# Kernel optimization log

Hardware: AMD Instinct MI355X
Metric: run time of the kernel (lower is better)

The kernel has to match this reference:

```python
import jax, jax.numpy as jnp
import numpy as np

B, N, C = 4, 1024, 1024
H = 16
D = C // H
FF = 4 * C
EPS = 1e-5


def setup_inputs() -> dict:
    key = jax.random.key(0)
    ks = jax.random.split(key, 16)
    s = 0.02
    return {
        "x": jax.random.normal(ks[0], (B, N, C), jnp.float32),
        "c": jax.random.normal(ks[1], (B, C), jnp.float32),
        "node_mask": jax.random.randint(ks[2], (B, N), 0, 2) > 0,
        "qkv_w": jax.random.normal(ks[3], (C, 3 * C), jnp.float32) * s,
        "proj_w": jax.random.normal(ks[4], (C, C), jnp.float32) * s,
        "proj_b": jnp.zeros((C,), jnp.float32),
        "fc1_w": jax.random.normal(ks[5], (C, FF), jnp.float32) * s,
        "fc1_b": jnp.zeros((FF,), jnp.float32),
        "fc2_w": jax.random.normal(ks[6], (FF, C), jnp.float32) * s,
        "fc2_b": jnp.zeros((C,), jnp.float32),
        "ada1_w": jax.random.normal(ks[7], (C, C), jnp.float32) * s,
        "ada1_b": jnp.zeros((C,), jnp.float32),
        "ada2_w": jax.random.normal(ks[8], (C, 6 * C), jnp.float32) * s,
        "ada2_b": jnp.zeros((6 * C,), jnp.float32),
    }


def _layernorm(x):
    # LayerNorm without affine params (elementwise_affine=False), eps=1e-5
    mu = jnp.mean(x, axis=-1, keepdims=True)
    var = jnp.mean(jnp.square(x - mu), axis=-1, keepdims=True)
    return (x - mu) * jax.lax.rsqrt(var + EPS)


def _modulate(x, shift, scale):
    return x * (1.0 + scale[:, None, :]) + shift[:, None, :]


def _attention(x, node_mask, qkv_w, proj_w, proj_b):
    b, n, c = x.shape
    qkv = (x @ qkv_w).reshape(b, n, 3, H, D)
    q, k, v = jnp.moveaxis(qkv, 2, 0)          # each [b, n, H, D]
    q = q.transpose(0, 2, 1, 3)                # [b, H, n, D]
    k = k.transpose(0, 2, 1, 3)
    v = v.transpose(0, 2, 1, 3)
    scale = D ** -0.5
    scores = jnp.einsum("bhnd,bhmd->bhnm", q, k) * scale
    mask = node_mask[:, None, None, :]          # key mask [b,1,1,n]
    scores = jnp.where(mask, scores, -jnp.inf)
    attn = jax.nn.softmax(scores, axis=-1)
    out = jnp.einsum("bhnm,bhmd->bhnd", attn, v)
    out = out.transpose(0, 2, 1, 3).reshape(b, n, c)
    return out @ proj_w + proj_b


def _mlp(x, fc1_w, fc1_b, fc2_w, fc2_b):
    h = jax.nn.gelu(x @ fc1_w + fc1_b, approximate=False)
    return h @ fc2_w + fc2_b


def reference(x, c, node_mask, qkv_w, proj_w, proj_b, fc1_w, fc1_b,
              fc2_w, fc2_b, ada1_w, ada1_b, ada2_w, ada2_b):
    # adaLN: Linear -> SiLU -> Linear -> 6 chunks along feature dim
    ada = jax.nn.silu(c @ ada1_w + ada1_b) @ ada2_w + ada2_b
    (shift_msa, scale_msa, gate_msa,
     shift_mlp, scale_mlp, gate_mlp) = jnp.split(ada, 6, axis=1)

    attn_out = _attention(x, node_mask, qkv_w, proj_w, proj_b)
    x = x + gate_msa[:, None, :] * _modulate(_layernorm(attn_out), shift_msa, scale_msa)

    mlp_out = _mlp(x, fc1_w, fc1_b, fc2_w, fc2_b)
    x = x + gate_mlp[:, None, :] * _modulate(_layernorm(mlp_out), shift_mlp, scale_mlp)
    return x
```

## Files before the change

kernel.cpp:

```cpp
#include <hip/hip_runtime.h>

typedef unsigned short u16;
typedef __attribute__((ext_vector_type(8))) short short8;
typedef __attribute__((ext_vector_type(8))) unsigned short u16x8;
typedef __attribute__((ext_vector_type(4))) unsigned short u16x4;
typedef __attribute__((ext_vector_type(4))) float f32x4;

#define DEVINL __device__ __forceinline__
#define SGB0 __builtin_amdgcn_sched_barrier(0)

DEVINL u16 f2b(float f) {
    union { float f; unsigned u; } a; a.f = f;
    unsigned r = a.u + 0x7FFFu + ((a.u >> 16) & 1u);
    return (u16)(r >> 16);
}
DEVINL float b2f(u16 h) {
    union { unsigned u; float f; } a; a.u = ((unsigned)h) << 16;
    return a.f;
}

DEVINL void gload16(const void* g, void* l) {
    __builtin_amdgcn_global_load_lds(
        (const __attribute__((address_space(1))) void*)g,
        (__attribute__((address_space(3))) void*)l, 16, 0, 0);
}

__global__ void detect_mask(const unsigned char* __restrict__ m, int nbytes, int* __restrict__ flag) {
    __shared__ int any;
    if (threadIdx.x == 0) any = 0;
    __syncthreads();
    int loc = 0;
    for (int i = threadIdx.x; i < nbytes; i += 256)
        if ((i & 3) && m[i]) loc = 1;
    if (loc) atomicOr(&any, 1);
    __syncthreads();
    if (threadIdx.x == 0) *flag = any;
}

__global__ __launch_bounds__(256) void f32_to_bf16(const float* __restrict__ in, u16* __restrict__ out, int n4) {
    int i = blockIdx.x * 256 + threadIdx.x;
    if (i >= n4) return;
    float4 v = ((const float4*)in)[i];
    u16x4 o = { f2b(v.x), f2b(v.y), f2b(v.z), f2b(v.w) };
    *(u16x4*)(out + (size_t)i * 4) = o;
}

__global__ __launch_bounds__(256) void transpose_bf16(const float* __restrict__ W, u16* __restrict__ WT, int K, int N) {
    __shared__ float tile[32][33];
    int tx = threadIdx.x, ty = threadIdx.y;
    int n0 = blockIdx.x * 32, k0 = blockIdx.y * 32;
#pragma unroll
    for (int i = 0; i < 4; i++)
        tile[ty + i * 8][tx] = W[(size_t)(k0 + ty + i * 8) * N + n0 + tx];
    __syncthreads();
#pragma unroll
    for (int i = 0; i < 4; i++)
        WT[(size_t)(n0 + ty + i * 8) * K + k0 + tx] = f2b(tile[tx][ty + i * 8]);
}

__global__ __launch_bounds__(256) void transpose_v(const u16* __restrict__ qkv, u16* __restrict__ vtg) {
    __shared__ u16 tile[64][72];
    const int bh = blockIdx.x & 63, nt = blockIdx.x >> 6;
    const int b = bh >> 4, h = bh & 15;
    const int t = threadIdx.x;
    const int r = t >> 3, c = (t & 7) << 3;
#pragma unroll
    for (int i = 0; i < 2; i++) {
        int rr = r + i * 32;
        *(u16x8*)&tile[rr][c] =
            *(const u16x8*)&qkv[(size_t)(b * 1024 + nt * 64 + rr) * 3072 + 2048 + h * 64 + c];
    }
    __syncthreads();
#pragma unroll
    for (int i = 0; i < 2; i++) {
        int d = r + i * 32;
        u16x8 o;
#pragma unroll
        for (int e = 0; e < 8; e++) o[e] = tile[c + e][d];
        *(u16x8*)&vtg[(size_t)bh * 65536 + (size_t)d * 1024 + nt * 64 + c] = o;
    }
}

template <int KRLOG2>
__global__ __launch_bounds__(256) void gemv_partial(
    const float* __restrict__ h, const float* __restrict__ w,
    float* __restrict__ part, int N, int K) {
    constexpr int KR = 1 << KRLOG2;
    constexpr int KR4 = KR >> 2;
    __shared__ float hs[4 * KR];
    __shared__ float red[256 * 16];
    const int t = threadIdx.x, wv = t >> 6, l = t & 63;
    const int j4 = blockIdx.x * 256 + l * 4;
    const int kb = blockIdx.y << KRLOG2;
    for (int idx = t; idx < 4 * KR; idx += 256) {
        int b = idx >> KRLOG2, kk = idx & (KR - 1);
        hs[idx] = h[b * K + kb + kk];
    }
    __syncthreads();
    float acc[4][4];
#pragma unroll
    for (int b = 0; b < 4; b++)
#pragma unroll
        for (int c = 0; c < 4; c++) acc[b][c] = 0.f;
    const float* wp = w + (size_t)(kb + wv * KR4) * N + j4;
#pragma unroll
    for (int i = 0; i < KR4; i++) {
        float4 wf = *(const float4*)(wp + (size_t)i * N);
        int kk = wv * KR4 + i;
#pragma unroll
        for (int b = 0; b < 4; b++) {
            float hv = hs[(b << KRLOG2) + kk];
            acc[b][0] += hv * wf.x;
            acc[b][1] += hv * wf.y;
            acc[b][2] += hv * wf.z;
            acc[b][3] += hv * wf.w;
        }
    }
#pragma unroll
    for (int b = 0; b < 4; b++)
#pragma unroll
        for (int c = 0; c < 4; c++)
            red[t * 16 + b * 4 + c] = acc[b][c];
    __syncthreads();
    if (t < 64) {
#pragma unroll
        for (int b = 0; b < 4; b++) {
            float4 s;
            s.x = red[l * 16 + b * 4 + 0] + red[(l + 64) * 16 + b * 4 + 0] + red[(l + 128) * 16 + b * 4 + 0] + red[(l + 192) * 16 + b * 4 + 0];
            s.y = red[l * 16 + b * 4 + 1] + red[(l + 64) * 16 + b * 4 + 1] + red[(l + 128) * 16 + b * 4 + 1] + red[(l + 192) * 16 + b * 4 + 1];
            s.z = red[l * 16 + b * 4 + 2] + red[(l + 64) * 16 + b * 4 + 2] + red[(l + 128) * 16 + b * 4 + 2] + red[(l + 192) * 16 + b * 4 + 2];
            s.w = red[l * 16 + b * 4 + 3] + red[(l + 64) * 16 + b * 4 + 3] + red[(l + 128) * 16 + b * 4 + 3] + red[(l + 192) * 16 + b * 4 + 3];
            *(float4*)&part[(size_t)(blockIdx.y * 4 + b) * N + j4] = s;
        }
    }
}

template <int SILU>
__global__ __launch_bounds__(256) void gemv_reduce(
    const float* __restrict__ part, const float* __restrict__ bias,
    float* __restrict__ out, int N, int NK) {
    int gid = blockIdx.x * 256 + threadIdx.x;
    int b = gid / N, j = gid - b * N;
    float s = bias[j];
    for (int i = 0; i < NK; i++) s += part[(size_t)(i * 4 + b) * N + j];
    if (SILU) s = s / (1.f + __expf(-s));
    out[gid] = s;
}

template <int EPI>
__global__ __launch_bounds__(256) void gemm_bt64(
    const u16* __restrict__ A, const u16* __restrict__ B, const float* __restrict__ bias,
    float* __restrict__ Cf, u16* __restrict__ Cb, int M, int N, int lda, int Ksub) {
    __shared__ u16 As[2][8192];
    __shared__ u16 Bs[2][8192];
    const int t = threadIdx.x;
    const int w = t >> 6, l = t & 63;
    const int l15 = l & 15, lg = l >> 4;
    const int nTN = N >> 7;
    const int ntiles = (M >> 7) * nTN;
    const int sk = blockIdx.x / ntiles;
    int tb = blockIdx.x - sk * ntiles;
    tb = (tb & 7) * (ntiles >> 3) + (tb >> 3);
    const int tm = tb / nTN, tn = tb - tm * nTN;
    const int row0 = tm << 7, col0 = tn << 7;
    const int wr = (w >> 1) << 6, wc = (w & 1) << 6;
    const int k_begin = sk * Ksub;

    const int rA = t >> 3;
    const int cswz = ((t & 7) ^ (rA & 7)) << 3;
    const u16* gA = A + (size_t)(row0 + rA) * lda + cswz + k_begin;
    const u16* gB = B + (size_t)(col0 + rA) * lda + cswz + k_begin;
    const int rsw = l15 & 7;

    f32x4 acc[4][4];
#pragma unroll
    for (int i = 0; i < 4; i++)
#pragma unroll
        for (int j = 0; j < 4; j++) acc[i][j] = (f32x4){0.f, 0.f, 0.f, 0.f};

    const int nsteps = Ksub >> 6;

#pragma unroll
    for (int j = 0; j < 4; j++) {
        gload16(gA + (size_t)j * 32 * lda, As[0] + j * 2048 + w * 512);
        gload16(gB + (size_t)j * 32 * lda, Bs[0] + j * 2048 + w * 512);
    }
#pragma unroll
    for (int j = 0; j < 4; j++) {
        gload16(gA + (size_t)j * 32 * lda + 64, As[1] + j * 2048 + w * 512);
        gload16(gB + (size_t)j * 32 * lda + 64, Bs[1] + j * 2048 + w * 512);
    }
    asm volatile("s_waitcnt vmcnt(8)" ::: "memory");
    SGB0;
    __builtin_amdgcn_s_barrier();
    SGB0;

    for (int it = 0; it < nsteps; ++it) {
        const int cur = it & 1;
        short8 af[2][4], bfr[2][4];
#pragma unroll
        for (int ks = 0; ks < 2; ks++) {
            const int chunk = ((ks << 2) + lg) ^ rsw;
#pragma unroll
            for (int mi = 0; mi < 4; mi++)
                af[ks][mi] = *(const short8*)&As[cur][((wr + mi * 16 + l15) << 6) + (chunk << 3)];
#pragma unroll
            for (int ni = 0; ni < 4; ni++)
                bfr[ks][ni] = *(const short8*)&Bs[cur][((wc + ni * 16 + l15) << 6) + (chunk << 3)];
        }
        asm volatile("s_waitcnt lgkmcnt(0)" ::: "memory");
        SGB0;
        __builtin_amdgcn_s_barrier();
        SGB0;
        if (it + 2 < nsteps) {
            const int k0 = (it + 2) << 6;
#pragma unroll
            for (int j = 0; j < 4; j++) {
                gload16(gA + (size_t)j * 32 * lda + k0, As[cur] + j * 2048 + w * 512);
                gload16(gB + (size_t)j * 32 * lda + k0, Bs[cur] + j * 2048 + w * 512);
            }
        }
        __builtin_amdgcn_s_setprio(1);
#pragma unroll
        for (int ks = 0; ks < 2; ks++)
#pragma unroll
            for (int mi = 0; mi < 4; mi++)
#pragma unroll
                for (int ni = 0; ni < 4; ni++)
                    acc[mi][ni] = __builtin_amdgcn_mfma_f32_16x16x32_bf16(af[ks][mi], bfr[ks][ni], acc[mi][ni], 0, 0, 0);
        __builtin_amdgcn_s_setprio(0);
        if (it + 1 < nsteps) {
            if (it + 2 < nsteps) asm volatile("s_waitcnt vmcnt(8)" ::: "memory");
            else                 asm volatile("s_waitcnt vmcnt(0)" ::: "memory");
            SGB0;
            __builtin_amdgcn_s_barrier();
            SGB0;
        }
    }

    float* Cfp = Cf ? Cf + (size_t)sk * M * N : nullptr;
    u16* Cbp = Cb ? Cb + (size_t)sk * M * N : nullptr;
#pragma unroll
    for (int mi = 0; mi < 4; mi++) {
#pragma unroll
        for (int ni = 0; ni < 4; ni++) {
#pragma unroll
            for (int j = 0; j < 4; j++) {
                int r = row0 + wr + mi * 16 + (lg << 2) + j;
                int c = col0 + wc + ni * 16 + l15;
                float v = acc[mi][ni][j];
                if (EPI == 0) {
                    Cbp[(size_t)r * N + c] = f2b(v);
                } else if (EPI == 2) {
                    float vv = v + bias[c];
                    float g = 0.5f * vv * (1.f + erff(vv * 0.70710678118f));
                    Cbp[(size_t)r * N + c] = f2b(g);
                } else {
                    Cfp[(size_t)r * N + c] = v;
                }
            }
        }
    }
}

__global__ __launch_bounds__(256) void attn_kernel(
    const u16* __restrict__ qkv, const u16* __restrict__ vtg,
    const unsigned char* __restrict__ maskb,
    const int* __restrict__ flagp, u16* __restrict__ out) {
    __shared__ u16 Qs[64 * 64];
    __shared__ u16 Ks[64 * 64];
    __shared__ u16 Vt[64 * 64];
    __shared__ u16 Ps[64 * 64];
    __shared__ float maskf[64];
    __shared__ float alpha_lds[64];
    __shared__ float lst_lds[64];

    int bi = (int)blockIdx.x;
    bi = (bi & 7) * 128 + (bi >> 3);
    const int qt = bi & 15, h = (bi >> 4) & 15, b = bi >> 8;
    const int t = threadIdx.x, w = t >> 6, l = t & 63;
    const int l15 = l & 15, lg = l >> 4;
    const int rsw = l15 & 7;
    const int flag = *flagp;
    const int q0 = qt << 6;
    const int bh = b * 16 + h;

    const int sr = t >> 3, sc = t & 7;
#pragma unroll
    for (int i = 0; i < 2; i++) {
        int r = sr + i * 32;
        u16x8 v = *(const u16x8*)&qkv[(size_t)(b * 1024 + q0 + r) * 3072 + h * 64 + sc * 8];
        u16x8 o;
#pragma unroll
        for (int e = 0; e < 8; e++) o[e] = f2b(b2f(v[e]) * 0.125f);
        *(u16x8*)&Qs[r * 64 + ((sc ^ (r & 7)) << 3)] = o;
    }

    f32x4 O[4];
#pragma unroll
    for (int nd = 0; nd < 4; nd++) O[nd] = (f32x4){0.f, 0.f, 0.f, 0.f};
    float mst = -1e30f, lst = 0.f;

    u16x8 kreg[2], vreg[2];
    float mnext;
    {
#pragma unroll
        for (int i = 0; i < 2; i++) {
            kreg[i] = *(const u16x8*)&qkv[(size_t)(b * 1024 + sr + i * 32) * 3072 + h * 64 + 1024 + sc * 8];
            vreg[i] = *(const u16x8*)&vtg[(size_t)bh * 65536 + (size_t)(sr + i * 32) * 1024 + sc * 8];
        }
        int gi = b * 1024 + (t & 63);
        bool ms = flag ? (maskb[gi] != 0) : (((const int*)maskb)[gi] != 0);
        mnext = ms ? 1.f : 0.f;
    }

    for (int kt = 0; kt < 16; kt++) {
        __syncthreads();
#pragma unroll
        for (int i = 0; i < 2; i++) {
            int r = sr + i * 32;
            *(u16x8*)&Ks[r * 64 + ((sc ^ (r & 7)) << 3)] = kreg[i];
            *(u16x8*)&Vt[r * 64 + ((sc ^ (r & 7)) << 3)] = vreg[i];
        }
        if (t < 64) maskf[t] = mnext;
        __syncthreads();
        if (kt < 15) {
            const int kn = (kt + 1) << 6;
#pragma unroll
            for (int i = 0; i < 2; i++) {
                kreg[i] = *(const u16x8*)&qkv[(size_t)(b * 1024 + kn + sr + i * 32) * 3072 + h * 64 + 1024 + sc * 8];
                vreg[i] = *(const u16x8*)&vtg[(size_t)bh * 65536 + (size_t)(sr + i * 32) * 1024 + kn + sc * 8];
            }
            int gi = b * 1024 + kn + (t & 63);
            bool ms = flag ? (maskb[gi] != 0) : (((const int*)maskb)[gi] != 0);
            mnext = ms ? 1.f : 0.f;
        }

        f32x4 S[4];
#pragma unroll
        for (int mi = 0; mi < 4; mi++) S[mi] = (f32x4){0.f, 0.f, 0.f, 0.f};
        __builtin_amdgcn_s_setprio(1);
#pragma unroll
        for (int ks = 0; ks < 2; ks++) {
            const int chunk = (((ks << 2) + lg) ^ rsw) << 3;
            short8 bq = *(const short8*)&Qs[(w * 16 + l15) * 64 + chunk];
#pragma unroll
            for (int mi = 0; mi < 4; mi++) {
                short8 ak = *(const short8*)&Ks[(mi * 16 + l15) * 64 + chunk];
                S[mi] = __builtin_amdgcn_mfma_f32_16x16x32_bf16(ak, bq, S[mi], 0, 0, 0);
            }
        }
        __builtin_amdgcn_s_setprio(0);

        float pm = -1e30f;
#pragma unroll
        for (int mi = 0; mi < 4; mi++) {
            f32x4 mk = *(const f32x4*)&maskf[mi * 16 + (lg << 2)];
#pragma unroll
            for (int j = 0; j < 4; j++) {
                float xv = (mk[j] > 0.f) ? S[mi][j] : -1e30f;
                S[mi][j] = xv;
                pm = fmaxf(pm, xv);
            }
        }
        pm = fmaxf(pm, __shfl_xor(pm, 16));
        pm = fmaxf(pm, __shfl_xor(pm, 32));

        bool skip = __all(pm <= mst + 8.f);
        float alpha = 1.f;
        if (!skip) {
            float mn = fmaxf(mst, pm);
            alpha = __expf(mst - mn);
            mst = mn;
        }

        float psum = 0.f;
        const int prow = w * 16 + l15;
#pragma unroll
        for (int mi = 0; mi < 4; mi++) {
            f32x4 mk = *(const f32x4*)&maskf[mi * 16 + (lg << 2)];
            u16x4 v4;
#pragma unroll
            for (int j = 0; j < 4; j++) {
                float p = __expf(S[mi][j] - mst) * mk[j];
                psum += p;
                v4[j] = f2b(p);
            }
            int ch = ((mi * 2 + (lg >> 1)) ^ rsw);
            *(u16x4*)&Ps[prow * 64 + (ch << 3) + ((lg & 1) << 2)] = v4;
        }
        psum += __shfl_xor(psum, 16);
        psum += __shfl_xor(psum, 32);
        lst = lst * alpha + psum;

        if (!skip) {
            if (lg == 0) alpha_lds[w * 16 + l15] = alpha;
            f32x4 af = *(const f32x4*)&alpha_lds[w * 16 + (lg << 2)];
#pragma unroll
            for (int nd = 0; nd < 4; nd++)
#pragma unroll
                for (int j = 0; j < 4; j++) O[nd][j] *= af[j];
        }

        __builtin_amdgcn_s_setprio(1);
#pragma unroll
        for (int ks = 0; ks < 2; ks++) {
            const int chunk = (((ks << 2) + lg) ^ rsw) << 3;
            short8 pa = *(const short8*)&Ps[(w * 16 + l15) * 64 + chunk];
#pragma unroll
            for (int nd = 0; nd < 4; nd++) {
                short8 bv = *(const short8*)&Vt[(nd * 16 + l15) * 64 + chunk];
                O[nd] = __builtin_amdgcn_mfma_f32_16x16x32_bf16(pa, bv, O[nd], 0, 0, 0);
            }
        }
        __builtin_amdgcn_s_setprio(0);
    }

    if (lg == 0) lst_lds[w * 16 + l15] = lst;
    f32x4 lf = *(const f32x4*)&lst_lds[w * 16 + (lg << 2)];
#pragma unroll
    for (int nd = 0; nd < 4; nd++)
#pragma unroll
        for (int j = 0; j < 4; j++) {
            int r = b * 1024 + q0 + w * 16 + (lg << 2) + j;
            int c = h * 64 + nd * 16 + l15;
            out[(size_t)r * 1024 + c] = f2b(O[nd][j] / lf[j]);
        }
}

template <int BF>
__global__ __launch_bounds__(256) void ln_mod_res2(
    const void* __restrict__ s0, const void* __restrict__ s1, const float* __restrict__ bias,
    const float* __restrict__ resid, const float* __restrict__ ada, int oS, int oC, int oG,
    float* __restrict__ outf, u16* __restrict__ outb) {
    __shared__ float red[8];
    const int row = blockIdx.x, t = threadIdx.x, b = row >> 10;
    const float4 bv = ((const float4*)bias)[t];
    float4 v;
    if (BF) {
        u16x4 a0 = *(const u16x4*)((const u16*)s0 + (size_t)row * 1024 + t * 4);
        u16x4 a1 = *(const u16x4*)((const u16*)s1 + (size_t)row * 1024 + t * 4);
        v.x = b2f(a0[0]) + b2f(a1[0]) + bv.x;
        v.y = b2f(a0[1]) + b2f(a1[1]) + bv.y;
        v.z = b2f(a0[2]) + b2f(a1[2]) + bv.z;
        v.w = b2f(a0[3]) + b2f(a1[3]) + bv.w;
    } else {
        float4 a0 = ((const float4*)((const float*)s0 + (size_t)row * 1024))[t];
        float4 a1 = ((const float4*)((const float*)s1 + (size_t)row * 1024))[t];
        v.x = a0.x + a1.x + bv.x;
        v.y = a0.y + a1.y + bv.y;
        v.z = a0.z + a1.z + bv.z;
        v.w = a0.w + a1.w + bv.w;
    }
    float s = v.x + v.y + v.z + v.w;
    float q = v.x * v.x + v.y * v.y + v.z * v.z + v.w * v.w;
#pragma unroll
    for (int off = 32; off >= 1; off >>= 1) {
        s += __shfl_down(s, off);
        q += __shfl_down(q, off);
    }
    if ((t & 63) == 0) { red[(t >> 6) * 2] = s; red[(t >> 6) * 2 + 1] = q; }
    __syncthreads();
    float sum = red[0] + red[2] + red[4] + red[6];
    float sq = red[1] + red[3] + red[5] + red[7];
    float mu = sum * (1.f / 1024.f);
    float var = sq * (1.f / 1024.f) - mu * mu;
    float rinv = rsqrtf(var + 1e-5f);
    const float* ad = ada + b * 6144;
    const float4 rv = ((const float4*)(resid + (size_t)row * 1024))[t];
    const float4 sc = ((const float4*)(ad + oC))[t];
    const float4 sh = ((const float4*)(ad + oS))[t];
    const float4 gt = ((const float4*)(ad + oG))[t];
    float4 o;
    o.x = rv.x + gt.x * ((v.x - mu) * rinv * (1.f + sc.x) + sh.x);
    o.y = rv.y + gt.y * ((v.y - mu) * rinv * (1.f + sc.y) + sh.y);
    o.z = rv.z + gt.z * ((v.z - mu) * rinv * (1.f + sc.z) + sh.z);
    o.w = rv.w + gt.w * ((v.w - mu) * rinv * (1.f + sc.w) + sh.w);
    ((float4*)(outf + (size_t)row * 1024))[t] = o;
    if (outb) {
        u16x4 ob = { f2b(o.x), f2b(o.y), f2b(o.z), f2b(o.w) };
        *(u16x4*)(outb + (size_t)row * 1024 + t * 4) = ob;
    }
}

extern "C" void kernel_launch(void* const* d_in, const int* in_sizes, int n_in,
                              void* d_out, int out_size, void* d_ws, size_t ws_size,
                              hipStream_t stream) {
    (void)in_sizes; (void)n_in; (void)out_size; (void)ws_size;
    const float* x = (const float*)d_in[0];
    const float* cvec = (const float*)d_in[1];
    const unsigned char* maskb = (const unsigned char*)d_in[2];
    const float* qkv_w = (const float*)d_in[3];
    const float* proj_w = (const float*)d_in[4];
    const float* proj_b = (const float*)d_in[5];
    const float* fc1_w = (const float*)d_in[6];
    const float* fc1_b = (const float*)d_in[7];
    const float* fc2_w = (const float*)d_in[8];
    const float* fc2_b = (const float*)d_in[9];
    const float* ada1_w = (const float*)d_in[10];
    const float* ada1_b = (const float*)d_in[11];
    const float* ada2_w = (const float*)d_in[12];
    const float* ada2_b = (const float*)d_in[13];
    float* outp = (float*)d_out;

    char* ws = (char*)d_ws;
    size_t off = 0;
    auto nxt = [&](size_t bytes) { size_t r = off; off += (bytes + 255) & ~(size_t)255; return r; };
    u16* qkvwT  = (u16*)(ws + nxt(3072ull * 1024 * 2));
    u16* projwT = (u16*)(ws + nxt(1024ull * 1024 * 2));
    u16* fc1wT  = (u16*)(ws + nxt(4096ull * 1024 * 2));
    u16* fc2wT  = (u16*)(ws + nxt(1024ull * 4096 * 2));
    float* adah = (float*)(ws + nxt(4ull * 1024 * 4));
    float* ada  = (float*)(ws + nxt(4ull * 6144 * 4));
    float* part1 = (float*)(ws + nxt(32ull * 4 * 1024 * 4));
    float* part2 = (float*)(ws + nxt(8ull * 4 * 6144 * 4));
    int* flag   = (int*)(ws + nxt(256));
    u16* xbf = (u16*)(ws + nxt(4096ull * 1024 * 2));
    u16* attn_buf = xbf;
    char* regC = ws + nxt(2ull * 4096 * 1024 * 4);
    u16* qkvbf = (u16*)regC;
    float* projpart = (float*)regC;
    u16* hbuf = (u16*)regC;
    float* y1 = (float*)(ws + nxt(4096ull * 1024 * 4));
    u16* y1b = (u16*)(ws + nxt(4096ull * 1024 * 2));
    u16* fc2part = (u16*)(ws + nxt(2ull * 4096 * 1024 * 2));
    u16* vtg = fc2part;

    detect_mask<<<1, 256, 0, stream>>>(maskb, 4096, flag);
    f32_to_bf16<<<4096, 256, 0, stream>>>(x, xbf, 1048576);
    transpose_bf16<<<dim3(96, 32), dim3(32, 8), 0, stream>>>(qkv_w, qkvwT, 1024, 3072);
    transpose_bf16<<<dim3(32, 32), dim3(32, 8), 0, stream>>>(proj_w, projwT, 1024, 1024);
    transpose_bf16<<<dim3(128, 32), dim3(32, 8), 0, stream>>>(fc1_w, fc1wT, 1024, 4096);
    transpose_bf16<<<dim3(32, 128), dim3(32, 8), 0, stream>>>(fc2_w, fc2wT, 4096, 1024);

    gemv_partial<5><<<dim3(4, 32), 256, 0, stream>>>(cvec, ada1_w, part1, 1024, 1024);
    gemv_reduce<1><<<16, 256, 0, stream>>>(part1, ada1_b, adah, 1024, 32);
    gemv_partial<7><<<dim3(24, 8), 256, 0, stream>>>(adah, ada2_w, part2, 6144, 1024);
    gemv_reduce<0><<<96, 256, 0, stream>>>(part2, ada2_b, ada, 6144, 8);

    gemm_bt64<0><<<768, 256, 0, stream>>>(xbf, qkvwT, nullptr, nullptr, qkvbf, 4096, 3072, 1024, 1024);
    transpose_v<<<1024, 256, 0, stream>>>(qkvbf, vtg);
    attn_kernel<<<1024, 256, 0, stream>>>(qkvbf, vtg, maskb, flag, attn_buf);
    gemm_bt64<3><<<512, 256, 0, stream>>>(attn_buf, projwT, nullptr, projpart, nullptr, 4096, 1024, 1024, 512);
    ln_mod_res2<0><<<4096, 256, 0, stream>>>(projpart, projpart + 4096ull * 1024, proj_b,
                                             x, ada, 0, 1024, 2048, y1, y1b);
    gemm_bt64<2><<<1024, 256, 0, stream>>>(y1b, fc1wT, fc1_b, nullptr, hbuf, 4096, 4096, 1024, 1024);
    gemm_bt64<0><<<512, 256, 0, stream>>>(hbuf, fc2wT, nullptr, nullptr, fc2part, 4096, 1024, 4096, 2048);
    ln_mod_res2<1><<<4096, 256, 0, stream>>>(fc2part, fc2part + 4096ull * 1024, fc2_b,
                                             y1, ada, 3072, 4096, 5120, outp, nullptr);
}
```

Measured before the change: 274.4 us.

## Add 256x256-tile 512-thread GEMM for QKV/FC1/FC2 with 4-way split-K FC2

Adds a new GEMM kernel with 256x256 output tiles, 8 waves per block and double-buffered direct-to-LDS loads, and uses it for the QKV, FC1 and FC2 matmuls in place of the 128x128 kernel. The larger tiles raise arithmetic intensity and cut global and LDS traffic per flop. FC2 now splits K four ways instead of two, writing two extra bf16 partial buffers into the start of the workspace, and the final LN kernel sums four partials. In exchange the kernel uses much more LDS and registers per block, launches fewer blocks (192–256, close to the CU count), which may underfill the GPU or hurt occupancy, and reusing workspace offset 0 risks aliasing with the weight buffers stored there.

```diff
diff --git a/kernel.cpp b/kernel.cpp
--- a/kernel.cpp
+++ b/kernel.cpp
@@ -145,6 +145,129 @@
     for (int i = 0; i < NK; i++) s += part[(size_t)(i * 4 + b) * N + j];
     if (SILU) s = s / (1.f + __expf(-s));
     out[gid] = s;
+}
+
+template <int EPI>
+__global__ __launch_bounds__(512) void gemm256(
+    const u16* __restrict__ A, const u16* __restrict__ B, const float* __restrict__ bias,
+    u16* __restrict__ Cb, u16* __restrict__ Cb2, int M, int N, int lda, int Ksub) {
+    __shared__ u16 As[2][256 * 64];
+    __shared__ u16 Bs[2][256 * 64];
+    const int t = threadIdx.x;
+    const int w = t >> 6, l = t & 63;
+    const int l15 = l & 15, lg = l >> 4;
+    const int nTN = N >> 8;
+    const int ntiles = (M >> 8) * nTN;
+    const int sk = blockIdx.x / ntiles;
+    int tb = blockIdx.x - sk * ntiles;
+    tb = (tb & 7) * (ntiles >> 3) + (tb >> 3);
+    const int tm = tb / nTN, tn = tb - tm * nTN;
+    const int row0 = tm << 8, col0 = tn << 8;
+    const int wr = (w >> 2) << 7, wc = (w & 3) << 6;
+    const int k_begin = sk * Ksub;
+
+    const int rA = t >> 3;
+    const int cswz = ((t & 7) ^ (rA & 7)) << 3;
+    const u16* gA = A + (size_t)(row0 + rA) * lda + cswz + k_begin;
+    const u16* gB = B + (size_t)(col0 + rA) * lda + cswz + k_begin;
+    const int rsw = l15 & 7;
+
+    f32x4 acc[8][4];
+#pragma unroll
+    for (int i = 0; i < 8; i++)
+#pragma unroll
+        for (int j = 0; j < 4; j++) acc[i][j] = (f32x4){0.f, 0.f, 0.f, 0.f};
+
+    const int nkt = Ksub >> 6;
+
+    auto STAGE = [&](int kt, int s) {
+        const int k0 = kt << 6;
+#pragma unroll
+        for (int j = 0; j < 4; j++)
+            gload16(gA + (size_t)j * 64 * lda + k0, As[s] + j * 4096 + w * 512);
+#pragma unroll
+        for (int j = 0; j < 4; j++)
+            gload16(gB + (size_t)j * 64 * lda + k0, Bs[s] + j * 4096 + w * 512);
+    };
+
+    STAGE(0, 0);
+    STAGE(1, 1);
+    asm volatile("s_waitcnt vmcnt(8)" ::: "memory");
+    SGB0;
+    __builtin_amdgcn_s_barrier();
+    SGB0;
+
+    for (int it = 0; it < nkt; ++it) {
+        const int cur = it & 1;
+        short8 af0[8], bf0[4];
+        {
+            const int chunk = (lg ^ rsw) << 3;
+#pragma unroll
+            for (int mi = 0; mi < 8; mi++)
+                af0[mi] = *(const short8*)&As[cur][((wr + mi * 16 + l15) << 6) + chunk];
+#pragma unroll
+            for (int ni = 0; ni < 4; ni++)
+                bf0[ni] = *(const short8*)&Bs[cur][((wc + ni * 16 + l15) << 6) + chunk];
+        }
+        __builtin_amdgcn_s_setprio(1);
+#pragma unroll
+        for (int mi = 0; mi < 8; mi++)
+#pragma unroll
+            for (int ni = 0; ni < 4; ni++)
+                acc[mi][ni] = __builtin_amdgcn_mfma_f32_16x16x32_bf16(af0[mi], bf0[ni], acc[mi][ni], 0, 0, 0);
+        __builtin_amdgcn_s_setprio(0);
+        short8 af1[8], bf1[4];
+        {
+            const int chunk = ((4 + lg) ^ rsw) << 3;
+#pragma unroll
+            for (int mi = 0; mi < 8; mi++)
+                af1[mi] = *(const short8*)&As[cur][((wr + mi * 16 + l15) << 6) + chunk];
+#pragma unroll
+            for (int ni = 0; ni < 4; ni++)
+                bf1[ni] = *(const short8*)&Bs[cur][((wc + ni * 16 + l15) << 6) + chunk];
+        }
+        asm volatile("s_waitcnt lgkmcnt(0)" ::: "memory");
+        SGB0;
+        __builtin_amdgcn_s_barrier();
+        SGB0;
+        if (it + 2 < nkt) STAGE(it + 2, cur);
+        __builtin_amdgcn_s_setprio(1);
+#pragma unroll
+        for (int mi = 0; mi < 8; mi++)
+#pragma unroll
+            for (int ni = 0; ni < 4; ni++)
+                acc[mi][ni] = __builtin_amdgcn_mfma_f32_16x16x32_bf16(af1[mi], bf1[ni], acc[mi][ni], 0, 0, 0);
+        __builtin_amdgcn_s_setprio(0);
+        if (it + 1 < nkt) {
+            if (it + 2 < nkt) asm volatile("s_waitcnt vmcnt(8)" ::: "memory");
+            else              asm volatile("s_waitcnt vmcnt(0)" ::: "memory");
+            SGB0;
+            __builtin_amdgcn_s_barrier();
+            SGB0;
+        }
+    }
+
+    const size_t MNsz = (size_t)M * N;
+    u16* dst = (sk < 2) ? Cb + (size_t)sk * MNsz : Cb2 + (size_t)(sk - 2) * MNsz;
+#pragma unroll
+    for (int mi = 0; mi < 8; mi++) {
+#pragma unroll
+        for (int ni = 0; ni < 4; ni++) {
+#pragma unroll
+            for (int j = 0; j < 4; j++) {
+                int r = row0 + wr + mi * 16 + (lg << 2) + j;
+                int c = col0 + wc + ni * 16 + l15;
+                float v = acc[mi][ni][j];
+                if (EPI == 0) {
+                    dst[(size_t)r * N + c] = f2b(v);
+                } else {
+                    float vv = v + bias[c];
+                    float g = 0.5f * vv * (1.f + erff(vv * 0.70710678118f));
+                    dst[(size_t)r * N + c] = f2b(g);
+                }
+            }
+        }
+    }
 }
 
 template <int EPI>
@@ -179,7 +302,6 @@
         for (int j = 0; j < 4; j++) acc[i][j] = (f32x4){0.f, 0.f, 0.f, 0.f};
 
     const int nsteps = Ksub >> 6;
-
 #pragma unroll
     for (int j = 0; j < 4; j++) {
         gload16(gA + (size_t)j * 32 * lda, As[0] + j * 2048 + w * 512);
@@ -438,12 +560,17 @@
     const float4 bv = ((const float4*)bias)[t];
     float4 v;
     if (BF) {
-        u16x4 a0 = *(const u16x4*)((const u16*)s0 + (size_t)row * 1024 + t * 4);
-        u16x4 a1 = *(const u16x4*)((const u16*)s1 + (size_t)row * 1024 + t * 4);
-        v.x = b2f(a0[0]) + b2f(a1[0]) + bv.x;
-        v.y = b2f(a0[1]) + b2f(a1[1]) + bv.y;
-        v.z = b2f(a0[2]) + b2f(a1[2]) + bv.z;
-        v.w = b2f(a0[3]) + b2f(a1[3]) + bv.w;
+        const size_t MN = 1ull << 22;
+        const u16* p0 = (const u16*)s0 + (size_t)row * 1024 + t * 4;
+        const u16* p1 = (const u16*)s1 + (size_t)row * 1024 + t * 4;
+        u16x4 a0 = *(const u16x4*)p0;
+        u16x4 a1 = *(const u16x4*)(p0 + MN);
+        u16x4 a2 = *(const u16x4*)p1;
+        u16x4 a3 = *(const u16x4*)(p1 + MN);
+        v.x = (b2f(a0[0]) + b2f(a1[0])) + (b2f(a2[0]) + b2f(a3[0])) + bv.x;
+        v.y = (b2f(a0[1]) + b2f(a1[1])) + (b2f(a2[1]) + b2f(a3[1])) + bv.y;
+        v.z = (b2f(a0[2]) + b2f(a1[2])) + (b2f(a2[2]) + b2f(a3[2])) + bv.z;
+        v.w = (b2f(a0[3]) + b2f(a1[3])) + (b2f(a2[3]) + b2f(a3[3])) + bv.w;
     } else {
         float4 a0 = ((const float4*)((const float*)s0 + (size_t)row * 1024))[t];
         float4 a1 = ((const float4*)((const float*)s1 + (size_t)row * 1024))[t];
@@ -525,6 +652,7 @@
     u16* y1b = (u16*)(ws + nxt(4096ull * 1024 * 2));
     u16* fc2part = (u16*)(ws + nxt(2ull * 4096 * 1024 * 2));
     u16* vtg = fc2part;
+    u16* fc2partB = (u16*)ws;
 
     detect_mask<<<1, 256, 0, stream>>>(maskb, 4096, flag);
     f32_to_bf16<<<4096, 256, 0, stream>>>(x, xbf, 1048576);
@@ -538,14 +666,14 @@
     gemv_partial<7><<<dim3(24, 8), 256, 0, stream>>>(adah, ada2_w, part2, 6144, 1024);
     gemv_reduce<0><<<96, 256, 0, stream>>>(part2, ada2_b, ada, 6144, 8);
 
-    gemm_bt64<0><<<768, 256, 0, stream>>>(xbf, qkvwT, nullptr, nullptr, qkvbf, 4096, 3072, 1024, 1024);
+    gemm256<0><<<192, 512, 0, stream>>>(xbf, qkvwT, nullptr, qkvbf, nullptr, 4096, 3072, 1024, 1024);
     transpose_v<<<1024, 256, 0, stream>>>(qkvbf, vtg);
     attn_kernel<<<1024, 256, 0, stream>>>(qkvbf, vtg, maskb, flag, attn_buf);
     gemm_bt64<3><<<512, 256, 0, stream>>>(attn_buf, projwT, nullptr, projpart, nullptr, 4096, 1024, 1024, 512);
     ln_mod_res2<0><<<4096, 256, 0, stream>>>(projpart, projpart + 4096ull * 1024, proj_b,
                                              x, ada, 0, 1024, 2048, y1, y1b);
-    gemm_bt64<2><<<1024, 256, 0, stream>>>(y1b, fc1wT, fc1_b, nullptr, hbuf, 4096, 4096, 1024, 1024);
-    gemm_bt64<0><<<512, 256, 0, stream>>>(hbuf, fc2wT, nullptr, nullptr, fc2part, 4096, 1024, 4096, 2048);
-    ln_mod_res2<1><<<4096, 256, 0, stream>>>(fc2part, fc2part + 4096ull * 1024, fc2_b,
+    gemm256<2><<<256, 512, 0, stream>>>(y1b, fc1wT, fc1_b, hbuf, nullptr, 4096, 4096, 1024, 1024);
+    gemm256<0><<<256, 512, 0, stream>>>(hbuf, fc2wT, nullptr, fc2part, fc2partB, 4096, 1024, 4096, 1024);
+    ln_mod_res2<1><<<4096, 256, 0, stream>>>(fc2part, fc2partB, fc2_b,
                                              y1, ada, 3072, 4096, 5120, outp, nullptr);
 }
```

Result: faster. 266.5 us (-2.9%).
